# Kernel optimization log

Hardware: AMD Instinct MI355X
Metric: run time of the kernel (lower is better)

## Reference

```python
import jax, jax.numpy as jnp
import numpy as np

B, T, K, H = 2, 4096, 512, 8


def setup_inputs() -> dict:
    key = jax.random.key(0)
    ks = jax.random.split(key, 6)
    scale = 1.0 / np.sqrt(K)
    return {
        "x": jax.random.normal(ks[0], (B, T, K), dtype=jnp.float32),
        "padding_mask": jnp.ones((B, T), dtype=jnp.int32),
        "Wq": jax.random.normal(ks[1], (K, K), dtype=jnp.float32) * scale,
        "Wk": jax.random.normal(ks[2], (K, K), dtype=jnp.float32) * scale,
        "Wv": jax.random.normal(ks[3], (K, K), dtype=jnp.float32) * scale,
        "Wu": jax.random.normal(ks[4], (K, K), dtype=jnp.float32) * scale,
        "bu": jnp.zeros((K,), dtype=jnp.float32),
    }


def reference(x, padding_mask, Wq, Wk, Wv, Wu, bu):
    b, t, e = x.shape
    h = H
    s = e // h
    # torch Linear: y = x @ W.T
    q = (x @ Wq.T).reshape(b, t, h, s).transpose(0, 2, 1, 3)  # (b,h,t,s)
    k = (x @ Wk.T).reshape(b, t, h, s).transpose(0, 2, 1, 3)
    v = (x @ Wv.T).reshape(b, t, h, s).transpose(0, 2, 1, 3)
    inv4 = e ** (-0.25)
    q = q * inv4
    k = k * inv4
    dot = jnp.einsum("bhqs,bhks->bhqk", q, k)  # (b,h,t,t)
    neg_inf = jnp.float32(-jnp.inf)
    # causal mask (self.mask == True)
    causal = jnp.triu(jnp.ones((t, t), dtype=bool), k=1)
    dot = jnp.where(causal[None, None], neg_inf, dot)
    # padding mask applied along the QUERY dimension, as in the original
    dot = jnp.where(padding_mask[:, None, :, None] == 0, neg_inf, dot)
    attn = jax.nn.softmax(dot, axis=-1)
    out = jnp.einsum("bhqk,bhks->bhqs", attn, v)  # (b,h,t,s)
    out = out.transpose(0, 2, 1, 3).reshape(b, t, e)
    return out @ Wu.T + bu
```

## Files before the change

kernel.cpp:

```cpp
#include <hip/hip_runtime.h>
#include <hip/hip_bf16.h>

#define BB 2
#define TT 4096
#define KK 512
#define HH 8
#define SS 64
#define MM 8192

typedef __attribute__((ext_vector_type(8))) short bf16x8;
typedef __attribute__((ext_vector_type(4))) float f32x4;
typedef unsigned int u32;
typedef __attribute__((ext_vector_type(2))) u32 u32x2;
typedef __attribute__((ext_vector_type(4))) u32 u32x4;

#define SCL_QK 0.25250488f

static __device__ __forceinline__ u32 cvt2(float lo, float hi) {
    u32 r;
    asm("v_cvt_pk_bf16_f32 %0, %1, %2" : "=v"(r) : "v"(lo), "v"(hi));
    return r;
}

#define GLOAD16(g, l) __builtin_amdgcn_global_load_lds( \
    (const __attribute__((address_space(1))) void*)(g), \
    (__attribute__((address_space(3))) void*)(l), 16, 0, 0)

static __device__ __forceinline__ int rho(int v) {
    return (v & 0x23) | ((v & 0x04) << 2) | ((v & 0x18) >> 1);
}

__global__ __launch_bounds__(256) void cvt_bf16(
    const float* __restrict__ x,
    const float* __restrict__ Wq, const float* __restrict__ Wk,
    const float* __restrict__ Wv, const float* __restrict__ Wu,
    short* __restrict__ xb, short* __restrict__ wb)
{
    const int NX = MM * KK;
    const int NW = KK * KK;
    int idx = blockIdx.x * blockDim.x + threadIdx.x;
    int total = (NX + 4 * NW) >> 3;
    for (int g = idx; g < total; g += gridDim.x * blockDim.x) {
        int e = g << 3;
        const float* src; short* dst; float scl = 1.0f;
        if (e < NX) { src = x + e; dst = xb + e; }
        else {
            int gg = e - NX;
            int wsel = gg >> 18;
            int off = gg & (NW - 1);
            src = (wsel == 0 ? Wq : wsel == 1 ? Wk : wsel == 2 ? Wv : Wu) + off;
            dst = wb + gg;
            if (wsel <= 1) scl = SCL_QK;
        }
        float4 a = *(const float4*)src;
        float4 b = *(const float4*)(src + 4);
        a.x *= scl; a.y *= scl; a.z *= scl; a.w *= scl;
        b.x *= scl; b.y *= scl; b.z *= scl; b.w *= scl;
        u32x4 wv = { cvt2(a.x, a.y), cvt2(a.z, a.w), cvt2(b.x, b.y), cvt2(b.z, b.w) };
        *(u32x4*)dst = wv;
    }
}

__global__ __launch_bounds__(256) void proj_qkv(
    const short* __restrict__ xb, const short* __restrict__ wb,
    short* __restrict__ q, short* __restrict__ k, short* __restrict__ v)
{
    __shared__ short aS[128 * 64];
    __shared__ short bS[128 * 64];
    int nt = blockIdx.x, mt = blockIdx.y, z = blockIdx.z;
    const short* W = wb + (size_t)z * KK * KK;
    short* dst = (z == 0) ? q : ((z == 1) ? k : v);
    bool tr = (z != 2);
    int tid = threadIdx.x, wave = tid >> 6, lane = tid & 63;
    int lr = lane & 15, lg = lane >> 4;
    int wr = wave >> 1, wc = wave & 1;
    int l8 = lane >> 3, c8 = lane & 7;

    const short* Ag = xb + (size_t)(mt * 128) * KK;
    const short* Bg = W + (size_t)(nt * 128) * KK;

    f32x4 acc[4][4];
#pragma unroll
    for (int m = 0; m < 4; ++m)
#pragma unroll
        for (int n = 0; n < 4; ++n) acc[m][n] = (f32x4){0.f, 0.f, 0.f, 0.f};

    for (int k0 = 0; k0 < KK; k0 += 64) {
        __syncthreads();
#pragma unroll
        for (int i = 0; i < 4; ++i) {
            int row = wave * 32 + i * 8 + l8;
            GLOAD16(Ag + (size_t)row * KK + k0 + c8 * 8, &aS[(wave * 32 + i * 8) * 64]);
            GLOAD16(Bg + (size_t)row * KK + k0 + c8 * 8, &bS[(wave * 32 + i * 8) * 64]);
        }
        __syncthreads();
#pragma unroll
        for (int kc = 0; kc < 2; ++kc) {
            bf16x8 af[4], bw[4];
#pragma unroll
            for (int m = 0; m < 4; ++m)
                af[m] = *(const bf16x8*)&aS[(wr * 64 + m * 16 + lr) * 64 + kc * 32 + lg * 8];
#pragma unroll
            for (int n = 0; n < 4; ++n)
                bw[n] = *(const bf16x8*)&bS[(wc * 64 + n * 16 + lr) * 64 + kc * 32 + lg * 8];
            if (tr) {
#pragma unroll
                for (int m = 0; m < 4; ++m)
#pragma unroll
                    for (int n = 0; n < 4; ++n)
                        acc[m][n] = __builtin_amdgcn_mfma_f32_16x16x32_bf16(bw[n], af[m], acc[m][n], 0, 0, 0);
            } else {
#pragma unroll
                for (int m = 0; m < 4; ++m)
#pragma unroll
                    for (int n = 0; n < 4; ++n)
                        acc[m][n] = __builtin_amdgcn_mfma_f32_16x16x32_bf16(af[m], bw[n], acc[m][n], 0, 0, 0);
            }
        }
    }

    if (tr) {
        int h = nt * 2 + wc;
#pragma unroll
        for (int n = 0; n < 4; ++n) {
            int s0 = n * 16 + lg * 4;
#pragma unroll
            for (int m = 0; m < 4; ++m) {
                int tg = mt * 128 + wr * 64 + m * 16 + lr;
                int b = tg >> 12, t = tg & (TT - 1);
                u32x2 pk = { cvt2(acc[m][n][0], acc[m][n][1]), cvt2(acc[m][n][2], acc[m][n][3]) };
                *(u32x2*)&dst[((size_t)(b * HH + h) * TT + t) * SS + s0] = pk;
            }
        }
    } else {
#pragma unroll
        for (int n = 0; n < 4; ++n) {
            int nn = nt * 128 + wc * 64 + n * 16 + lr;
            int h = nn >> 6, s = nn & 63;
#pragma unroll
            for (int m = 0; m < 4; ++m) {
                int m0 = mt * 128 + wr * 64 + m * 16 + lg * 4;
                int b = m0 >> 12, t0 = m0 & (TT - 1);
                u32x2 pk = { cvt2(acc[m][n][0], acc[m][n][1]), cvt2(acc[m][n][2], acc[m][n][3]) };
                *(u32x2*)&dst[(((size_t)(b * HH + h)) * SS + s) * TT + t0] = pk;
            }
        }
    }
}

__global__ __launch_bounds__(256) void proj_out(
    const short* __restrict__ a, const short* __restrict__ Wub,
    const float* __restrict__ bu, float* __restrict__ out)
{
    __shared__ short aS[64 * 64];
    __shared__ short bS[128 * 64];
    int nt = blockIdx.x, mt = blockIdx.y;
    int tid = threadIdx.x, wave = tid >> 6, lane = tid & 63;
    int lr = lane & 15, lg = lane >> 4;
    int wr = wave >> 1, wc = wave & 1;
    int l8 = lane >> 3, c8 = lane & 7;

    const short* Ag = a + (size_t)(mt * 64) * KK;
    const short* Bg = Wub + (size_t)(nt * 128) * KK;

    f32x4 acc[2][4];
#pragma unroll
    for (int m = 0; m < 2; ++m)
#pragma unroll
        for (int n = 0; n < 4; ++n) acc[m][n] = (f32x4){0.f, 0.f, 0.f, 0.f};

    for (int k0 = 0; k0 < KK; k0 += 64) {
        __syncthreads();
#pragma unroll
        for (int i = 0; i < 2; ++i) {
            int row = wave * 16 + i * 8 + l8;
            GLOAD16(Ag + (size_t)row * KK + k0 + c8 * 8, &aS[(wave * 16 + i * 8) * 64]);
        }
#pragma unroll
        for (int i = 0; i < 4; ++i) {
            int row = wave * 32 + i * 8 + l8;
            GLOAD16(Bg + (size_t)row * KK + k0 + c8 * 8, &bS[(wave * 32 + i * 8) * 64]);
        }
        __syncthreads();
#pragma unroll
        for (int kc = 0; kc < 2; ++kc) {
            bf16x8 af[2], bw[4];
#pragma unroll
            for (int m = 0; m < 2; ++m)
                af[m] = *(const bf16x8*)&aS[(wr * 32 + m * 16 + lr) * 64 + kc * 32 + lg * 8];
#pragma unroll
            for (int n = 0; n < 4; ++n)
                bw[n] = *(const bf16x8*)&bS[(wc * 64 + n * 16 + lr) * 64 + kc * 32 + lg * 8];
#pragma unroll
            for (int m = 0; m < 2; ++m)
#pragma unroll
                for (int n = 0; n < 4; ++n)
                    acc[m][n] = __builtin_amdgcn_mfma_f32_16x16x32_bf16(bw[n], af[m], acc[m][n], 0, 0, 0);
        }
    }

#pragma unroll
    for (int n = 0; n < 4; ++n) {
        int f0 = nt * 128 + wc * 64 + n * 16 + lg * 4;
        float4 bias4 = *(const float4*)&bu[f0];
#pragma unroll
        for (int m = 0; m < 2; ++m) {
            int t = mt * 64 + wr * 32 + m * 16 + lr;
            float4 ov = { acc[m][n][0] + bias4.x, acc[m][n][1] + bias4.y,
                          acc[m][n][2] + bias4.z, acc[m][n][3] + bias4.w };
            *(float4*)&out[(size_t)t * KK + f0] = ov;
        }
    }
}

__global__ __launch_bounds__(256) void flash_attn(
    const short* __restrict__ Q, const short* __restrict__ Kv,
    const short* __restrict__ Vt, short* __restrict__ Oout)
{
    __shared__ short k_lds[64][72];
    __shared__ short v_lds[64][72];

    int u = blockIdx.x;
    int xcd = u & 7, sblk = u >> 3;
    int bh = 2 * xcd + (sblk & 1);
    int i4 = sblk >> 1;
    int qt = (i4 < 16) ? (63 - i4) : (i4 < 32 ? (i4 - 16) : (i4 < 48 ? (79 - i4) : (i4 - 32)));

    int tid = threadIdx.x, wave = tid >> 6, lane = tid & 63;
    int lr = lane & 15, lg = lane >> 4;
    int b = bh >> 3, h = bh & 7;

    const short* Qb = Q + (size_t)bh * TT * SS;
    const short* Kb = Kv + (size_t)bh * TT * SS;
    const short* Vb = Vt + (size_t)bh * SS * TT;

    int urow = tid >> 3, useg = tid & 7;
    int kdr0 = rho(urow), kdr1 = rho(urow + 32);

    int qrow0 = qt * 64 + wave * 16;

    bf16x8 a_q[2];
#pragma unroll
    for (int kc = 0; kc < 2; ++kc)
        a_q[kc] = *(const bf16x8*)&Qb[(size_t)(qrow0 + lr) * SS + kc * 32 + lg * 8];

    f32x4 o[4];
#pragma unroll
    for (int n = 0; n < 4; ++n) o[n] = (f32x4){0.f, 0.f, 0.f, 0.f};
    float m_run = -INFINITY, l_run = 0.f;

    int nkv = qt + 1;
    bf16x8 kr0, kr1, vr0, vr1;
    kr0 = *(const bf16x8*)&Kb[(size_t)urow * SS + useg * 8];
    kr1 = *(const bf16x8*)&Kb[(size_t)(urow + 32) * SS + useg * 8];
    vr0 = *(const bf16x8*)&Vb[(size_t)urow * TT + useg * 8];
    vr1 = *(const bf16x8*)&Vb[(size_t)(urow + 32) * TT + useg * 8];

    for (int kt = 0; kt < nkv; ++kt) {
        __syncthreads();
        *(bf16x8*)&k_lds[kdr0][useg * 8]      = kr0;
        *(bf16x8*)&k_lds[kdr1][useg * 8]      = kr1;
        *(bf16x8*)&v_lds[urow][useg * 8]      = vr0;
        *(bf16x8*)&v_lds[urow + 32][useg * 8] = vr1;
        if (kt + 1 < nkv) {
            int kn = kt + 1;
            kr0 = *(const bf16x8*)&Kb[(size_t)(kn * 64 + urow) * SS + useg * 8];
            kr1 = *(const bf16x8*)&Kb[(size_t)(kn * 64 + urow + 32) * SS + useg * 8];
            vr0 = *(const bf16x8*)&Vb[(size_t)urow * TT + kn * 64 + useg * 8];
            vr1 = *(const bf16x8*)&Vb[(size_t)(urow + 32) * TT + kn * 64 + useg * 8];
        }
        __syncthreads();

        f32x4 sc[4];
#pragma unroll
        for (int ct = 0; ct < 4; ++ct) sc[ct] = (f32x4){0.f, 0.f, 0.f, 0.f};
        __builtin_amdgcn_s_setprio(1);
#pragma unroll
        for (int kc = 0; kc < 2; ++kc) {
#pragma unroll
            for (int ct = 0; ct < 4; ++ct) {
                bf16x8 kf = *(const bf16x8*)&k_lds[ct * 16 + lr][kc * 32 + lg * 8];
                sc[ct] = __builtin_amdgcn_mfma_f32_16x16x32_bf16(kf, a_q[kc], sc[ct], 0, 0, 0);
            }
        }
        __builtin_amdgcn_s_setprio(0);
        if (kt == qt) {
            int qq = qrow0 + lr;
#pragma unroll
            for (int ct = 0; ct < 4; ++ct) {
                int kv0 = kt * 64 + (ct >> 1) * 32 + lg * 8 + (ct & 1) * 4;
#pragma unroll
                for (int r = 0; r < 4; ++r)
                    if (kv0 + r > qq) sc[ct][r] = -INFINITY;
            }
        }
        float mx = -INFINITY;
#pragma unroll
        for (int ct = 0; ct < 4; ++ct)
#pragma unroll
            for (int r = 0; r < 4; ++r) mx = fmaxf(mx, sc[ct][r]);
        mx = fmaxf(mx, __shfl_xor(mx, 16));
        mx = fmaxf(mx, __shfl_xor(mx, 32));
        if (!__all(mx <= m_run + 8.0f)) {
            float mnew = fmaxf(m_run, mx);
            float corr = __builtin_amdgcn_exp2f(m_run - mnew);
            l_run *= corr;
#pragma unroll
            for (int st = 0; st < 4; ++st)
#pragma unroll
                for (int r = 0; r < 4; ++r) o[st][r] *= corr;
            m_run = mnew;
        }
        float s0 = 0.f;
#pragma unroll
        for (int ct = 0; ct < 4; ++ct)
#pragma unroll
            for (int r = 0; r < 4; ++r) {
                float pf = __builtin_amdgcn_exp2f(sc[ct][r] - m_run);
                sc[ct][r] = pf;
                s0 += pf;
            }
        s0 += __shfl_xor(s0, 16);
        s0 += __shfl_xor(s0, 32);
        l_run += s0;

        __builtin_amdgcn_s_setprio(1);
#pragma unroll
        for (int kc = 0; kc < 2; ++kc) {
            u32x4 pw = { cvt2(sc[2 * kc][0], sc[2 * kc][1]),
                         cvt2(sc[2 * kc][2], sc[2 * kc][3]),
                         cvt2(sc[2 * kc + 1][0], sc[2 * kc + 1][1]),
                         cvt2(sc[2 * kc + 1][2], sc[2 * kc + 1][3]) };
            bf16x8 pb = __builtin_bit_cast(bf16x8, pw);
#pragma unroll
            for (int st = 0; st < 4; ++st) {
                bf16x8 vf = *(const bf16x8*)&v_lds[st * 16 + lr][kc * 32 + lg * 8];
                o[st] = __builtin_amdgcn_mfma_f32_16x16x32_bf16(vf, pb, o[st], 0, 0, 0);
            }
        }
        __builtin_amdgcn_s_setprio(0);
    }

    float inv = 1.f / l_run;
    int t = qrow0 + lr;
#pragma unroll
    for (int st = 0; st < 4; ++st) {
        u32x2 ov = { cvt2(o[st][0] * inv, o[st][1] * inv), cvt2(o[st][2] * inv, o[st][3] * inv) };
        *(u32x2*)&Oout[(size_t)(b * TT + t) * KK + h * 64 + st * 16 + lg * 4] = ov;
    }
}

extern "C" void kernel_launch(void* const* d_in, const int* in_sizes, int n_in,
                              void* d_out, int out_size, void* d_ws, size_t ws_size,
                              hipStream_t stream) {
    const float* x  = (const float*)d_in[0];
    const float* Wq = (const float*)d_in[2];
    const float* Wk = (const float*)d_in[3];
    const float* Wv = (const float*)d_in[4];
    const float* Wu = (const float*)d_in[5];
    const float* bu = (const float*)d_in[6];
    float* out = (float*)d_out;

    short* q_ws  = (short*)d_ws;
    short* k_ws  = q_ws + (size_t)MM * KK;
    short* v_ws  = k_ws + (size_t)MM * KK;
    short* a_ws  = v_ws + (size_t)MM * KK;
    short* wb_ws = a_ws + (size_t)MM * KK;

    cvt_bf16<<<2560, 256, 0, stream>>>(x, Wq, Wk, Wv, Wu, a_ws, wb_ws);

    dim3 gQKV(KK / 128, MM / 128, 3);
    proj_qkv<<<gQKV, 256, 0, stream>>>(a_ws, wb_ws, q_ws, k_ws, v_ws);

    flash_attn<<<1024, 256, 0, stream>>>(q_ws, k_ws, v_ws, a_ws);

    dim3 gO(KK / 128, MM / 64);
    proj_out<<<gO, 256, 0, stream>>>(a_ws, wb_ws + 3 * (size_t)KK * KK, bu, out);
}
```

Baseline: 192.1 us.

## Split long causal query tiles across two blocks and double-buffer GEMM staging

New measurement: 197.4 us. +2.8%, slower.

```diff
diff --git a/kernel.cpp b/kernel.cpp
--- a/kernel.cpp
+++ b/kernel.cpp
@@ -65,8 +65,8 @@
     const short* __restrict__ xb, const short* __restrict__ wb,
     short* __restrict__ q, short* __restrict__ k, short* __restrict__ v)
 {
-    __shared__ short aS[128 * 64];
-    __shared__ short bS[128 * 64];
+    __shared__ short aS[2][128 * 32];
+    __shared__ short bS[2][128 * 32];
     int nt = blockIdx.x, mt = blockIdx.y, z = blockIdx.z;
     const short* W = wb + (size_t)z * KK * KK;
     short* dst = (z == 0) ? q : ((z == 1) ? k : v);
@@ -74,7 +74,7 @@
     int tid = threadIdx.x, wave = tid >> 6, lane = tid & 63;
     int lr = lane & 15, lg = lane >> 4;
     int wr = wave >> 1, wc = wave & 1;
-    int l8 = lane >> 3, c8 = lane & 7;
+    int sri = lane >> 2, ss0 = lane & 3;
 
     const short* Ag = xb + (size_t)(mt * 128) * KK;
     const short* Bg = W + (size_t)(nt * 128) * KK;
@@ -85,38 +85,47 @@
 #pragma unroll
         for (int n = 0; n < 4; ++n) acc[m][n] = (f32x4){0.f, 0.f, 0.f, 0.f};
 
-    for (int k0 = 0; k0 < KK; k0 += 64) {
+    auto STAGE = [&](int buf, int k0) {
+#pragma unroll
+        for (int g = 0; g < 2; ++g) {
+            int R0 = wave * 32 + g * 16;
+            int srow = R0 + sri;
+            int sseg = ss0 ^ ((srow >> 1) & 3);
+            GLOAD16(Ag + (size_t)srow * KK + k0 + sseg * 8, &aS[buf][R0 * 32]);
+            GLOAD16(Bg + (size_t)srow * KK + k0 + sseg * 8, &bS[buf][R0 * 32]);
+        }
+    };
+
+    STAGE(0, 0);
+    int cur = 0;
+    for (int kt = 0; kt < 16; ++kt) {
         __syncthreads();
-#pragma unroll
-        for (int i = 0; i < 4; ++i) {
-            int row = wave * 32 + i * 8 + l8;
-            GLOAD16(Ag + (size_t)row * KK + k0 + c8 * 8, &aS[(wave * 32 + i * 8) * 64]);
-            GLOAD16(Bg + (size_t)row * KK + k0 + c8 * 8, &bS[(wave * 32 + i * 8) * 64]);
-        }
-        __syncthreads();
-#pragma unroll
-        for (int kc = 0; kc < 2; ++kc) {
-            bf16x8 af[4], bw[4];
+        if (kt < 15) STAGE(cur ^ 1, (kt + 1) * 32);
+        bf16x8 af[4], bw[4];
+#pragma unroll
+        for (int m = 0; m < 4; ++m) {
+            int row = wr * 64 + m * 16 + lr;
+            af[m] = *(const bf16x8*)&aS[cur][row * 32 + (lg ^ ((row >> 1) & 3)) * 8];
+        }
+#pragma unroll
+        for (int n = 0; n < 4; ++n) {
+            int row = wc * 64 + n * 16 + lr;
+            bw[n] = *(const bf16x8*)&bS[cur][row * 32 + (lg ^ ((row >> 1) & 3)) * 8];
+        }
+        if (tr) {
 #pragma unroll
             for (int m = 0; m < 4; ++m)
-                af[m] = *(const bf16x8*)&aS[(wr * 64 + m * 16 + lr) * 64 + kc * 32 + lg * 8];
-#pragma unroll
-            for (int n = 0; n < 4; ++n)
-                bw[n] = *(const bf16x8*)&bS[(wc * 64 + n * 16 + lr) * 64 + kc * 32 + lg * 8];
-            if (tr) {
-#pragma unroll
-                for (int m = 0; m < 4; ++m)
-#pragma unroll
-                    for (int n = 0; n < 4; ++n)
-                        acc[m][n] = __builtin_amdgcn_mfma_f32_16x16x32_bf16(bw[n], af[m], acc[m][n], 0, 0, 0);
-            } else {
-#pragma unroll
-                for (int m = 0; m < 4; ++m)
-#pragma unroll
-                    for (int n = 0; n < 4; ++n)
-                        acc[m][n] = __builtin_amdgcn_mfma_f32_16x16x32_bf16(af[m], bw[n], acc[m][n], 0, 0, 0);
-            }
-        }
+#pragma unroll
+                for (int n = 0; n < 4; ++n)
+                    acc[m][n] = __builtin_amdgcn_mfma_f32_16x16x32_bf16(bw[n], af[m], acc[m][n], 0, 0, 0);
+        } else {
+#pragma unroll
+            for (int m = 0; m < 4; ++m)
+#pragma unroll
+                for (int n = 0; n < 4; ++n)
+                    acc[m][n] = __builtin_amdgcn_mfma_f32_16x16x32_bf16(af[m], bw[n], acc[m][n], 0, 0, 0);
+        }
+        cur ^= 1;
     }
 
     if (tr) {
@@ -152,13 +161,13 @@
     const short* __restrict__ a, const short* __restrict__ Wub,
     const float* __restrict__ bu, float* __restrict__ out)
 {
-    __shared__ short aS[64 * 64];
-    __shared__ short bS[128 * 64];
+    __shared__ short aS[2][64 * 32];
+    __shared__ short bS[2][128 * 32];
     int nt = blockIdx.x, mt = blockIdx.y;
     int tid = threadIdx.x, wave = tid >> 6, lane = tid & 63;
     int lr = lane & 15, lg = lane >> 4;
     int wr = wave >> 1, wc = wave & 1;
-    int l8 = lane >> 3, c8 = lane & 7;
+    int sri = lane >> 2, ss0 = lane & 3;
 
     const short* Ag = a + (size_t)(mt * 64) * KK;
     const short* Bg = Wub + (size_t)(nt * 128) * KK;
@@ -169,34 +178,44 @@
 #pragma unroll
         for (int n = 0; n < 4; ++n) acc[m][n] = (f32x4){0.f, 0.f, 0.f, 0.f};
 
-    for (int k0 = 0; k0 < KK; k0 += 64) {
+    auto STAGE = [&](int buf, int k0) {
+        {
+            int R0 = wave * 16;
+            int srow = R0 + sri;
+            int sseg = ss0 ^ ((srow >> 1) & 3);
+            GLOAD16(Ag + (size_t)srow * KK + k0 + sseg * 8, &aS[buf][R0 * 32]);
+        }
+#pragma unroll
+        for (int g = 0; g < 2; ++g) {
+            int R0 = wave * 32 + g * 16;
+            int srow = R0 + sri;
+            int sseg = ss0 ^ ((srow >> 1) & 3);
+            GLOAD16(Bg + (size_t)srow * KK + k0 + sseg * 8, &bS[buf][R0 * 32]);
+        }
+    };
+
+    STAGE(0, 0);
+    int cur = 0;
+    for (int kt = 0; kt < 16; ++kt) {
         __syncthreads();
-#pragma unroll
-        for (int i = 0; i < 2; ++i) {
-            int row = wave * 16 + i * 8 + l8;
-            GLOAD16(Ag + (size_t)row * KK + k0 + c8 * 8, &aS[(wave * 16 + i * 8) * 64]);
-        }
-#pragma unroll
-        for (int i = 0; i < 4; ++i) {
-            int row = wave * 32 + i * 8 + l8;
-            GLOAD16(Bg + (size_t)row * KK + k0 + c8 * 8, &bS[(wave * 32 + i * 8) * 64]);
-        }
-        __syncthreads();
-#pragma unroll
-        for (int kc = 0; kc < 2; ++kc) {
-            bf16x8 af[2], bw[4];
-#pragma unroll
-            for (int m = 0; m < 2; ++m)
-                af[m] = *(const bf16x8*)&aS[(wr * 32 + m * 16 + lr) * 64 + kc * 32 + lg * 8];
+        if (kt < 15) STAGE(cur ^ 1, (kt + 1) * 32);
+        bf16x8 af[2], bw[4];
+#pragma unroll
+        for (int m = 0; m < 2; ++m) {
+            int row = wr * 32 + m * 16 + lr;
+            af[m] = *(const bf16x8*)&aS[cur][row * 32 + (lg ^ ((row >> 1) & 3)) * 8];
+        }
+#pragma unroll
+        for (int n = 0; n < 4; ++n) {
+            int row = wc * 64 + n * 16 + lr;
+            bw[n] = *(const bf16x8*)&bS[cur][row * 32 + (lg ^ ((row >> 1) & 3)) * 8];
+        }
+#pragma unroll
+        for (int m = 0; m < 2; ++m)
 #pragma unroll
             for (int n = 0; n < 4; ++n)
-                bw[n] = *(const bf16x8*)&bS[(wc * 64 + n * 16 + lr) * 64 + kc * 32 + lg * 8];
-#pragma unroll
-            for (int m = 0; m < 2; ++m)
-#pragma unroll
-                for (int n = 0; n < 4; ++n)
-                    acc[m][n] = __builtin_amdgcn_mfma_f32_16x16x32_bf16(bw[n], af[m], acc[m][n], 0, 0, 0);
-        }
+                acc[m][n] = __builtin_amdgcn_mfma_f32_16x16x32_bf16(bw[n], af[m], acc[m][n], 0, 0, 0);
+        cur ^= 1;
     }
 
 #pragma unroll
@@ -215,16 +234,25 @@
 
 __global__ __launch_bounds__(256) void flash_attn(
     const short* __restrict__ Q, const short* __restrict__ Kv,
-    const short* __restrict__ Vt, short* __restrict__ Oout)
+    const short* __restrict__ Vt, short* __restrict__ Oout,
+    float* __restrict__ opart, float* __restrict__ mlws)
 {
     __shared__ short k_lds[64][72];
     __shared__ short v_lds[64][72];
 
     int u = blockIdx.x;
-    int xcd = u & 7, sblk = u >> 3;
-    int bh = 2 * xcd + (sblk & 1);
-    int i4 = sblk >> 1;
-    int qt = (i4 < 16) ? (63 - i4) : (i4 < 32 ? (i4 - 16) : (i4 < 48 ? (79 - i4) : (i4 - 32)));
+    int xcd = u & 7, r = u >> 3;
+    int bh = 2 * xcd + (r & 1);
+    int cc = (r >> 1) & 31;
+    int slot = r >> 6;
+    int qt, klo, khi;
+    if (slot == 0) { qt = cc; klo = 0; khi = cc + 1; }
+    else {
+        qt = 63 - cc;
+        int nkv = qt + 1, mid = (nkv + 1) >> 1;
+        klo = (slot == 1) ? 0 : mid;
+        khi = (slot == 1) ? mid : nkv;
+    }
 
     int tid = threadIdx.x, wave = tid >> 6, lane = tid & 63;
     int lr = lane & 15, lg = lane >> 4;
@@ -249,20 +277,19 @@
     for (int n = 0; n < 4; ++n) o[n] = (f32x4){0.f, 0.f, 0.f, 0.f};
     float m_run = -INFINITY, l_run = 0.f;
 
-    int nkv = qt + 1;
     bf16x8 kr0, kr1, vr0, vr1;
-    kr0 = *(const bf16x8*)&Kb[(size_t)urow * SS + useg * 8];
-    kr1 = *(const bf16x8*)&Kb[(size_t)(urow + 32) * SS + useg * 8];
-    vr0 = *(const bf16x8*)&Vb[(size_t)urow * TT + useg * 8];
-    vr1 = *(const bf16x8*)&Vb[(size_t)(urow + 32) * TT + useg * 8];
-
-    for (int kt = 0; kt < nkv; ++kt) {
+    kr0 = *(const bf16x8*)&Kb[(size_t)(klo * 64 + urow) * SS + useg * 8];
+    kr1 = *(const bf16x8*)&Kb[(size_t)(klo * 64 + urow + 32) * SS + useg * 8];
+    vr0 = *(const bf16x8*)&Vb[(size_t)urow * TT + klo * 64 + useg * 8];
+    vr1 = *(const bf16x8*)&Vb[(size_t)(urow + 32) * TT + klo * 64 + useg * 8];
+
+    for (int kt = klo; kt < khi; ++kt) {
         __syncthreads();
         *(bf16x8*)&k_lds[kdr0][useg * 8]      = kr0;
         *(bf16x8*)&k_lds[kdr1][useg * 8]      = kr1;
         *(bf16x8*)&v_lds[urow][useg * 8]      = vr0;
         *(bf16x8*)&v_lds[urow + 32][useg * 8] = vr1;
-        if (kt + 1 < nkv) {
+        if (kt + 1 < khi) {
             int kn = kt + 1;
             kr0 = *(const bf16x8*)&Kb[(size_t)(kn * 64 + urow) * SS + useg * 8];
             kr1 = *(const bf16x8*)&Kb[(size_t)(kn * 64 + urow + 32) * SS + useg * 8];
@@ -290,15 +317,15 @@
             for (int ct = 0; ct < 4; ++ct) {
                 int kv0 = kt * 64 + (ct >> 1) * 32 + lg * 8 + (ct & 1) * 4;
 #pragma unroll
-                for (int r = 0; r < 4; ++r)
-                    if (kv0 + r > qq) sc[ct][r] = -INFINITY;
+                for (int rr = 0; rr < 4; ++rr)
+                    if (kv0 + rr > qq) sc[ct][rr] = -INFINITY;
             }
         }
         float mx = -INFINITY;
 #pragma unroll
         for (int ct = 0; ct < 4; ++ct)
 #pragma unroll
-            for (int r = 0; r < 4; ++r) mx = fmaxf(mx, sc[ct][r]);
+            for (int rr = 0; rr < 4; ++rr) mx = fmaxf(mx, sc[ct][rr]);
         mx = fmaxf(mx, __shfl_xor(mx, 16));
         mx = fmaxf(mx, __shfl_xor(mx, 32));
         if (!__all(mx <= m_run + 8.0f)) {
@@ -308,16 +335,16 @@
 #pragma unroll
             for (int st = 0; st < 4; ++st)
 #pragma unroll
-                for (int r = 0; r < 4; ++r) o[st][r] *= corr;
+                for (int rr = 0; rr < 4; ++rr) o[st][rr] *= corr;
             m_run = mnew;
         }
         float s0 = 0.f;
 #pragma unroll
         for (int ct = 0; ct < 4; ++ct)
 #pragma unroll
-            for (int r = 0; r < 4; ++r) {
-                float pf = __builtin_amdgcn_exp2f(sc[ct][r] - m_run);
-                sc[ct][r] = pf;
+            for (int rr = 0; rr < 4; ++rr) {
+                float pf = __builtin_amdgcn_exp2f(sc[ct][rr] - m_run);
+                sc[ct][rr] = pf;
                 s0 += pf;
             }
         s0 += __shfl_xor(s0, 16);
@@ -341,12 +368,55 @@
         __builtin_amdgcn_s_setprio(0);
     }
 
-    float inv = 1.f / l_run;
-    int t = qrow0 + lr;
-#pragma unroll
-    for (int st = 0; st < 4; ++st) {
-        u32x2 ov = { cvt2(o[st][0] * inv, o[st][1] * inv), cvt2(o[st][2] * inv, o[st][3] * inv) };
-        *(u32x2*)&Oout[(size_t)(b * TT + t) * KK + h * 64 + st * 16 + lg * 4] = ov;
+    if (slot == 0) {
+        float inv = 1.f / l_run;
+        int t = qrow0 + lr;
+#pragma unroll
+        for (int st = 0; st < 4; ++st) {
+            u32x2 ov = { cvt2(o[st][0] * inv, o[st][1] * inv), cvt2(o[st][2] * inv, o[st][3] * inv) };
+            *(u32x2*)&Oout[(size_t)(b * TT + t) * KK + h * 64 + st * 16 + lg * 4] = ov;
+        }
+    } else {
+        int pidx = bh * 32 + (qt - 32);
+        float* ob = opart + ((size_t)(pidx * 2 + (slot - 1)) << 12);
+#pragma unroll
+        for (int st = 0; st < 4; ++st)
+            *(f32x4*)&ob[(wave * 16 + lr) * 64 + st * 16 + lg * 4] = o[st];
+        if (lg == 0) {
+            float* mlp = mlws + (size_t)(pidx * 2 + (slot - 1)) * 128;
+            mlp[wave * 16 + lr] = m_run;
+            mlp[64 + wave * 16 + lr] = l_run;
+        }
+    }
+}
+
+__global__ __launch_bounds__(64) void merge_halves(
+    const float* __restrict__ opart, const float* __restrict__ mlws,
+    short* __restrict__ Oout)
+{
+    int p = blockIdx.x;
+    int bh = p >> 5, qt = (p & 31) + 32;
+    int qq = threadIdx.x;
+    const float* ml0 = mlws + (size_t)(p * 2) * 128;
+    const float* ml1 = mlws + (size_t)(p * 2 + 1) * 128;
+    float m0 = ml0[qq], l0 = ml0[64 + qq];
+    float m1 = ml1[qq], l1 = ml1[64 + qq];
+    float m = fmaxf(m0, m1);
+    float c0 = __builtin_amdgcn_exp2f(m0 - m);
+    float c1 = __builtin_amdgcn_exp2f(m1 - m);
+    float inv = 1.f / (l0 * c0 + l1 * c1);
+    c0 *= inv; c1 *= inv;
+    const float* o0 = opart + (((size_t)(p * 2)) << 12) + qq * 64;
+    const float* o1 = opart + (((size_t)(p * 2 + 1)) << 12) + qq * 64;
+    int b = bh >> 3, h = bh & 7;
+    short* dst = Oout + ((size_t)(b * TT) + qt * 64 + qq) * KK + h * 64;
+#pragma unroll
+    for (int s4 = 0; s4 < 16; ++s4) {
+        float4 a0 = ((const float4*)o0)[s4];
+        float4 a1 = ((const float4*)o1)[s4];
+        u32x2 pk = { cvt2(a0.x * c0 + a1.x * c1, a0.y * c0 + a1.y * c1),
+                     cvt2(a0.z * c0 + a1.z * c1, a0.w * c0 + a1.w * c1) };
+        *(u32x2*)&dst[s4 * 4] = pk;
     }
 }
 
@@ -366,13 +436,17 @@
     short* v_ws  = k_ws + (size_t)MM * KK;
     short* a_ws  = v_ws + (size_t)MM * KK;
     short* wb_ws = a_ws + (size_t)MM * KK;
+    float* ml_ws = (float*)(wb_ws + 4 * (size_t)KK * KK);
+    float* opart = out;
 
     cvt_bf16<<<2560, 256, 0, stream>>>(x, Wq, Wk, Wv, Wu, a_ws, wb_ws);
 
     dim3 gQKV(KK / 128, MM / 128, 3);
     proj_qkv<<<gQKV, 256, 0, stream>>>(a_ws, wb_ws, q_ws, k_ws, v_ws);
 
-    flash_attn<<<1024, 256, 0, stream>>>(q_ws, k_ws, v_ws, a_ws);
+    flash_attn<<<1536, 256, 0, stream>>>(q_ws, k_ws, v_ws, a_ws, opart, ml_ws);
+
+    merge_halves<<<512, 64, 0, stream>>>(opart, ml_ws, a_ws);
 
     dim3 gO(KK / 128, MM / 64);
     proj_out<<<gO, 256, 0, stream>>>(a_ws, wb_ws + 3 * (size_t)KK * KK, bu, out);
```
